# Kernel tuning notes

Measured on AMD Instinct MI355X. Metric: run time of the kernel, lower is better.

## Reference

```python
import jax, jax.numpy as jnp
import numpy as np

N = 268  # nodes per graph (4288 / nhid=16)


def _cheb_norm(edge_index, edge_weight):
    # PyG ChebConv normalization with normalization='sym', lambda_max=2.0:
    # L_hat = (2/lambda_max) * L - I = -D^{-1/2} A D^{-1/2} (diagonal cancels to 0)
    row, col = edge_index[0], edge_index[1]
    deg = jax.ops.segment_sum(edge_weight, row, num_segments=N)
    dis = jnp.where(deg > 0, jax.lax.rsqrt(deg), 0.0)
    return -edge_weight * dis[row] * dis[col]


def _cheb_conv(x, edge_index, norm, w, b):
    # K=2: out = T0 @ W0 + T1 @ W1 + b,  T0 = x, T1 = L_hat x
    row, col = edge_index[0], edge_index[1]
    tx1 = jax.ops.segment_sum(norm[:, None] * x[col], row, num_segments=N)
    return x @ w[0] + tx1 @ w[1] + b


def _forward_single(x, edge_index, edge_attr, gc1_w, gc1_b, gc4_w, gc4_b):
    norm = _cheb_norm(edge_index, edge_attr)
    h = jax.nn.relu(_cheb_conv(x, edge_index, norm, gc1_w, gc1_b))
    # dropout in eval mode -> identity
    return _cheb_conv(h, edge_index, norm, gc4_w, gc4_b)  # [N, nhid]


def setup_inputs() -> dict:
    key = jax.random.key(0)
    ks = jax.random.split(key, 20)
    B, E, F, H = 64, 8576, 268, 16
    inp = {}
    for i, nm in enumerate(['x1', 'x2', 'x3']):
        inp[nm] = jax.random.normal(ks[i], (B, N, F), dtype=jnp.float32)
    for i, nm in enumerate(['edge_index1', 'edge_index2', 'edge_index3']):
        inp[nm] = jax.random.randint(ks[3 + i], (B, 2, E), 0, N)
    for i, nm in enumerate(['edge_attr1', 'edge_attr2', 'edge_attr3']):
        inp[nm] = jax.random.uniform(ks[6 + i], (B, E), dtype=jnp.float32)
    s = 0.05
    inp['gc1_w'] = jax.random.normal(ks[9], (2, F, H), dtype=jnp.float32) * s
    inp['gc1_b'] = jnp.zeros((H,), dtype=jnp.float32)
    inp['gc4_w'] = jax.random.normal(ks[10], (2, H, H), dtype=jnp.float32) * s
    inp['gc4_b'] = jnp.zeros((H,), dtype=jnp.float32)
    inp['fc1_w'] = jax.random.normal(ks[11], (1024, N * H), dtype=jnp.float32) * s
    inp['fc1_b'] = jnp.zeros((1024,), dtype=jnp.float32)
    inp['fc2_w'] = jax.random.normal(ks[12], (512, 1024), dtype=jnp.float32) * s
    inp['fc2_b'] = jnp.zeros((512,), dtype=jnp.float32)
    return inp


def reference(x1, x2, x3, edge_index1, edge_index2, edge_index3,
              edge_attr1, edge_attr2, edge_attr3,
              gc1_w, gc1_b, gc4_w, gc4_b, fc1_w, fc1_b, fc2_w, fc2_b):
    conv = jax.vmap(_forward_single, in_axes=(0, 0, 0, None, None, None, None))

    def branch(x, ei, ea):
        c = conv(x, ei, ea, gc1_w, gc1_b, gc4_w, gc4_b)      # [B, N, H]
        f = c.reshape(c.shape[0], -1)                        # [B, 4288]
        h = jax.nn.relu(f @ fc1_w.T + fc1_b)                 # classifier dropout: eval -> id
        return h @ fc2_w.T + fc2_b                           # [B, 512]

    return (branch(x1, edge_index1, edge_attr1),
            branch(x2, edge_index2, edge_attr2),
            branch(x3, edge_index3, edge_attr3))
```

## Files before the change

### kernel.cpp

```cpp
#include <hip/hip_runtime.h>


#define NN   268
#define EE   8576
#define NG   192
#define FDIM 4288
#define CONVT 1024

typedef __bf16 bf16_t;
typedef bf16_t bf16x8 __attribute__((ext_vector_type(8)));
typedef bf16_t bf16x4 __attribute__((ext_vector_type(4)));
typedef float  f32x4  __attribute__((ext_vector_type(4)));

#define WB_OFF   0
#define FB_OFF   2195456
#define WXT_OFF  (FB_OFF + 411648)
#define H1_OFF   (WXT_OFF + 4608)
#define R1P_OFF  (H1_OFF + 196608)
#define R2P_OFF  (R1P_OFF + 1572864)

#define NCASTB 2144

__global__ __launch_bounds__(256) void k_prep(
    const float* __restrict__ fc1w, const float* __restrict__ gc1w,
    bf16_t* __restrict__ wbf, bf16_t* __restrict__ wxt)
{
    if (blockIdx.x < NCASTB) {
        const int t = blockIdx.x * 256 + threadIdx.x;
        const int lane = t & 63;
        const int rest = t >> 6;
        const int n = (rest / 134) * 16 + (lane & 15);
        const int k = (rest % 134) * 32 + (lane >> 4) * 8;
        const float4 a = *(const float4*)(fc1w + (size_t)n * FDIM + k);
        const float4 b = *(const float4*)(fc1w + (size_t)n * FDIM + k + 4);
        bf16x8 v;
        v[0] = (bf16_t)a.x; v[1] = (bf16_t)a.y; v[2] = (bf16_t)a.z; v[3] = (bf16_t)a.w;
        v[4] = (bf16_t)b.x; v[5] = (bf16_t)b.y; v[6] = (bf16_t)b.z; v[7] = (bf16_t)b.w;
        *(bf16x8*)(wbf + (size_t)t * 8) = v;
    } else {
        for (int idx = threadIdx.x; idx < 2 * 9 * 64; idx += 256) {
            const int lane = idx & 63, chunk = (idx >> 6) % 9, nt = idx / (9 * 64);
            const int n = lane & 15, q = lane >> 4;
            bf16x8 v;
#pragma unroll
            for (int j = 0; j < 8; ++j) {
                const int k = chunk * 32 + q * 8 + j;
                v[j] = (k < NN) ? (bf16_t)gc1w[nt * FDIM + k * 16 + n] : (bf16_t)0.f;
            }
            *(bf16x8*)(wxt + (size_t)idx * 8) = v;
        }
    }
}

__global__ __launch_bounds__(CONVT) void k_conv(
    const float* __restrict__ x0, const float* __restrict__ x1, const float* __restrict__ x2,
    const int* __restrict__ ei0, const int* __restrict__ ei1, const int* __restrict__ ei2,
    const float* __restrict__ ea0, const float* __restrict__ ea1, const float* __restrict__ ea2,
    const bf16_t* __restrict__ wxt,
    const float* __restrict__ gc1b, const float* __restrict__ gc4w,
    const float* __restrict__ gc4b, bf16_t* __restrict__ fout)
{
    const int g = blockIdx.x;
    const int br = g >> 6, b = g & 63;
    const float* xg = ((br == 0) ? x0 : (br == 1) ? x1 : x2) + (size_t)b * (NN * NN);
    const int*   ei = (br == 0) ? ei0 : (br == 1) ? ei1 : ei2;
    const float* ea = (br == 0) ? ea0 : (br == 1) ? ea1 : ea2;
    const int*   rowp = ei + (size_t)b * (2 * EE);
    const int*   colp = rowp + EE;
    const float* eap  = ea + (size_t)b * EE;

    __shared__ unsigned int e_s[EE];
    __shared__ __align__(16) bf16_t A_s[FDIM];
    __shared__ __align__(16) bf16_t S_s[FDIM];
    __shared__ __align__(16) float  xw0_s[FDIM];
    __shared__ float degS[NN];
    __shared__ int   cntS[NN];
    __shared__ int   offS[NN + 1];
    __shared__ int   curS[NN];
    __shared__ float w4_s[512];
    __shared__ float b1_s[16];
    __shared__ float b4_s[16];
    const int tid = threadIdx.x;
    const int lane = tid & 63, wid = tid >> 6;

    if (tid < NN) { degS[tid] = 0.f; cntS[tid] = 0; }
    if (tid < 512) w4_s[tid] = gc4w[tid];
    if (tid < 16) { b1_s[tid] = gc1b[tid]; b4_s[tid] = gc4b[tid]; }

    {
        const int q = lane >> 4, nlo = lane & 15;
        for (int mt = wid; mt < 17; mt += 16) {
            const int mrow = mt * 16 + nlo;
            const bool mvalid = (mrow < NN);
            const float* xrow = xg + (size_t)mrow * NN;
            f32x4 acc0 = {0.f, 0.f, 0.f, 0.f}, acc1 = {0.f, 0.f, 0.f, 0.f};
            for (int ch = 0; ch < 9; ++ch) {
                const int k0 = ch * 32 + q * 8;
                float4 p0 = make_float4(0.f, 0.f, 0.f, 0.f);
                float4 p1 = make_float4(0.f, 0.f, 0.f, 0.f);
                if (mvalid) {
                    if (k0 < NN)     p0 = *(const float4*)(xrow + k0);
                    if (k0 + 4 < NN) p1 = *(const float4*)(xrow + k0 + 4);
                }
                bf16x8 a;
                a[0] = (bf16_t)p0.x; a[1] = (bf16_t)p0.y; a[2] = (bf16_t)p0.z; a[3] = (bf16_t)p0.w;
                a[4] = (bf16_t)p1.x; a[5] = (bf16_t)p1.y; a[6] = (bf16_t)p1.z; a[7] = (bf16_t)p1.w;
                const bf16x8 b0 = *(const bf16x8*)(wxt + (size_t)(ch * 64 + lane) * 8);
                const bf16x8 b1 = *(const bf16x8*)(wxt + (size_t)(576 + ch * 64 + lane) * 8);
                acc0 = __builtin_amdgcn_mfma_f32_16x16x32_bf16(a, b0, acc0, 0, 0, 0);
                acc1 = __builtin_amdgcn_mfma_f32_16x16x32_bf16(a, b1, acc1, 0, 0, 0);
            }
#pragma unroll
            for (int r = 0; r < 4; ++r) {
                const int row = mt * 16 + q * 4 + r;
                if (row < NN) {
                    xw0_s[row * 16 + nlo] = acc0[r];
                    A_s[row * 16 + nlo] = (bf16_t)acc1[r];
                }
            }
        }
    }
    __syncthreads();

    for (int e = tid; e < EE; e += CONVT) {
        const int r = rowp[e];
        atomicAdd(&degS[r], eap[e]);
        atomicAdd(&cntS[r], 1);
    }
    for (int st = 1; st < NN; st <<= 1) {
        __syncthreads();
        int v = 0;
        if (tid < NN) { v = cntS[tid]; if (tid >= st) v += cntS[tid - st]; }
        __syncthreads();
        if (tid < NN) cntS[tid] = v;
    }
    __syncthreads();
    if (tid < NN) offS[tid + 1] = cntS[tid];
    if (tid == 0) offS[0] = 0;
    __syncthreads();
    if (tid < NN) {
        curS[tid] = offS[tid];
        const float d = degS[tid];
        degS[tid] = (d > 0.f) ? rsqrtf(d) : 0.f;
    }
    __syncthreads();
    for (int e = tid; e < EE; e += CONVT) {
        const int r = rowp[e], c = colp[e];
        const float nv = -eap[e] * degS[r] * degS[c];
        union { float f; unsigned u; } cv; cv.f = nv;
        const unsigned bits = (cv.u + 0x7fffu + ((cv.u >> 16) & 1u)) >> 16;
        const int pos = atomicAdd(&curS[r], 1);
        e_s[pos] = ((unsigned)c << 16) | bits;
    }
    __syncthreads();

    const int j4 = tid & 3, nl = tid >> 2;
    const bf16x4* A4 = (const bf16x4*)A_s;

    for (int n = nl; n < NN; n += 256) {
        const int s = offS[n], e = offS[n + 1];
        const f32x4 xv = *(const f32x4*)&xw0_s[n * 16 + j4 * 4];
        float ax = 0.f, ay = 0.f, az = 0.f, aw = 0.f;
        int i = s;
        for (; i + 3 < e; i += 4) {
            const unsigned p0 = e_s[i], p1 = e_s[i + 1], p2 = e_s[i + 2], p3 = e_s[i + 3];
            const float w0 = __uint_as_float(p0 << 16);
            const float w1 = __uint_as_float(p1 << 16);
            const float w2 = __uint_as_float(p2 << 16);
            const float w3 = __uint_as_float(p3 << 16);
            const bf16x4 a0 = A4[(p0 >> 16) * 4 + j4];
            const bf16x4 a1 = A4[(p1 >> 16) * 4 + j4];
            const bf16x4 a2 = A4[(p2 >> 16) * 4 + j4];
            const bf16x4 a3 = A4[(p3 >> 16) * 4 + j4];
            ax += w0 * (float)a0[0] + w1 * (float)a1[0] + w2 * (float)a2[0] + w3 * (float)a3[0];
            ay += w0 * (float)a0[1] + w1 * (float)a1[1] + w2 * (float)a2[1] + w3 * (float)a3[1];
            az += w0 * (float)a0[2] + w1 * (float)a1[2] + w2 * (float)a2[2] + w3 * (float)a3[2];
            aw += w0 * (float)a0[3] + w1 * (float)a1[3] + w2 * (float)a2[3] + w3 * (float)a3[3];
        }
        for (; i < e; ++i) {
            const unsigned p0 = e_s[i];
            const float w0 = __uint_as_float(p0 << 16);
            const bf16x4 a0 = A4[(p0 >> 16) * 4 + j4];
            ax += w0 * (float)a0[0]; ay += w0 * (float)a0[1];
            az += w0 * (float)a0[2]; aw += w0 * (float)a0[3];
        }
        bf16x4 h;
        h[0] = (bf16_t)fmaxf(xv[0] + ax + b1_s[j4 * 4 + 0], 0.f);
        h[1] = (bf16_t)fmaxf(xv[1] + ay + b1_s[j4 * 4 + 1], 0.f);
        h[2] = (bf16_t)fmaxf(xv[2] + az + b1_s[j4 * 4 + 2], 0.f);
        h[3] = (bf16_t)fmaxf(xv[3] + aw + b1_s[j4 * 4 + 3], 0.f);
        *(bf16x4*)&S_s[n * 16 + j4 * 4] = h;
    }
    __syncthreads();

    for (int idx = tid; idx < FDIM; idx += CONVT) {
        const int n = idx >> 4, j = idx & 15;
        const bf16x8 s0 = *(const bf16x8*)&S_s[n * 16];
        const bf16x8 s1 = *(const bf16x8*)&S_s[n * 16 + 8];
        float a1 = 0.f;
#pragma unroll
        for (int k = 0; k < 8; ++k) a1 += (float)s0[k] * w4_s[256 + k * 16 + j];
#pragma unroll
        for (int k = 0; k < 8; ++k) a1 += (float)s1[k] * w4_s[256 + (k + 8) * 16 + j];
        A_s[idx] = (bf16_t)a1;
    }
    __syncthreads();

    for (int n = nl; n < NN; n += 256) {
        const int s = offS[n], e = offS[n + 1];
        float ax = 0.f, ay = 0.f, az = 0.f, aw = 0.f;
        int i = s;
        for (; i + 3 < e; i += 4) {
            const unsigned p0 = e_s[i], p1 = e_s[i + 1], p2 = e_s[i + 2], p3 = e_s[i + 3];
            const float w0 = __uint_as_float(p0 << 16);
            const float w1 = __uint_as_float(p1 << 16);
            const float w2 = __uint_as_float(p2 << 16);
            const float w3 = __uint_as_float(p3 << 16);
            const bf16x4 a0 = A4[(p0 >> 16) * 4 + j4];
            const bf16x4 a1 = A4[(p1 >> 16) * 4 + j4];
            const bf16x4 a2 = A4[(p2 >> 16) * 4 + j4];
            const bf16x4 a3 = A4[(p3 >> 16) * 4 + j4];
            ax += w0 * (float)a0[0] + w1 * (float)a1[0] + w2 * (float)a2[0] + w3 * (float)a3[0];
            ay += w0 * (float)a0[1] + w1 * (float)a1[1] + w2 * (float)a2[1] + w3 * (float)a3[1];
            az += w0 * (float)a0[2] + w1 * (float)a1[2] + w2 * (float)a2[2] + w3 * (float)a3[2];
            aw += w0 * (float)a0[3] + w1 * (float)a1[3] + w2 * (float)a2[3] + w3 * (float)a3[3];
        }
        for (; i < e; ++i) {
            const unsigned p0 = e_s[i];
            const float w0 = __uint_as_float(p0 << 16);
            const bf16x4 a0 = A4[(p0 >> 16) * 4 + j4];
            ax += w0 * (float)a0[0]; ay += w0 * (float)a0[1];
            az += w0 * (float)a0[2]; aw += w0 * (float)a0[3];
        }
        float h0[4];
#pragma unroll
        for (int c2 = 0; c2 < 4; ++c2) h0[c2] = b4_s[j4 * 4 + c2];
        const bf16x8 s0 = *(const bf16x8*)&S_s[n * 16];
        const bf16x8 s1 = *(const bf16x8*)&S_s[n * 16 + 8];
#pragma unroll
        for (int k = 0; k < 8; ++k) {
            const float sv = (float)s0[k];
#pragma unroll
            for (int c2 = 0; c2 < 4; ++c2) h0[c2] += sv * w4_s[k * 16 + j4 * 4 + c2];
        }
#pragma unroll
        for (int k = 0; k < 8; ++k) {
            const float sv = (float)s1[k];
#pragma unroll
            for (int c2 = 0; c2 < 4; ++c2) h0[c2] += sv * w4_s[(k + 8) * 16 + j4 * 4 + c2];
        }
        bf16x4 o;
        o[0] = (bf16_t)(h0[0] + ax); o[1] = (bf16_t)(h0[1] + ay);
        o[2] = (bf16_t)(h0[2] + az); o[3] = (bf16_t)(h0[3] + aw);
        *(bf16x4*)(fout + (size_t)g * FDIM + n * 16 + j4 * 4) = o;
    }
}

__global__ __launch_bounds__(256) void k_fc1(
    const bf16_t* __restrict__ fb, const bf16_t* __restrict__ wbf, float* __restrict__ r1p)
{
    const int mt = blockIdx.x, nb = blockIdx.y, kz = blockIdx.z;
    const int wid = threadIdx.x >> 6, lane = threadIdx.x & 63;
    const int q = lane >> 4, nlo = lane & 15;
    const int n0 = nb * 128 + wid * 32;
    const int cstart = kz * 17;
    const int ccnt   = (kz == 7) ? 15 : 17;

    const bf16_t* arow = fb + (size_t)(mt * 16 + nlo) * FDIM + q * 8;
    const int nt0 = nb * 8 + wid * 2;
    f32x4 acc[2];
#pragma unroll
    for (int t = 0; t < 2; ++t) { acc[t][0]=0.f; acc[t][1]=0.f; acc[t][2]=0.f; acc[t][3]=0.f; }

    for (int ch = 0; ch < ccnt; ++ch) {
        const size_t ko = (size_t)(cstart + ch) * 32;
        const bf16x8 a = *(const bf16x8*)(arow + ko);
#pragma unroll
        for (int t = 0; t < 2; ++t) {
            const bf16x8 bv = *(const bf16x8*)(
                wbf + (((size_t)(nt0 + t) * 134 + cstart + ch) * 64 + lane) * 8);
            acc[t] = __builtin_amdgcn_mfma_f32_16x16x32_bf16(a, bv, acc[t], 0, 0, 0);
        }
    }
    float* outp = r1p + (size_t)kz * (NG * 1024);
#pragma unroll
    for (int t = 0; t < 2; ++t)
#pragma unroll
        for (int r = 0; r < 4; ++r)
            outp[(size_t)(mt * 16 + q * 4 + r) * 1024 + n0 + t * 16 + nlo] = acc[t][r];
}

__global__ __launch_bounds__(256) void k_red1(
    const float* __restrict__ r1p, const float* __restrict__ b1, float* __restrict__ h1)
{
    const size_t i = ((size_t)blockIdx.x * 256 + threadIdx.x) * 4;
    const size_t S = (size_t)NG * 1024;
    float4 s = *(const float4*)(r1p + i);
#pragma unroll
    for (int k = 1; k < 8; ++k) {
        const float4 t = *(const float4*)(r1p + (size_t)k * S + i);
        s.x += t.x; s.y += t.y; s.z += t.z; s.w += t.w;
    }
    const float4 bb = *(const float4*)(b1 + (i & 1023));
    float4 o;
    o.x = fmaxf(s.x + bb.x, 0.f);
    o.y = fmaxf(s.y + bb.y, 0.f);
    o.z = fmaxf(s.z + bb.z, 0.f);
    o.w = fmaxf(s.w + bb.w, 0.f);
    *(float4*)(h1 + i) = o;
}

__global__ __launch_bounds__(256) void k_fc2(
    const float* __restrict__ h1, const float* __restrict__ w2, float* __restrict__ r2p)
{
    const int m0 = blockIdx.x * 64;
    const int n0 = blockIdx.y * 64;
    const int kb = blockIdx.z * 64;
    __shared__ float rs[64][68];
    __shared__ float wss[64][68];
    const int tid = threadIdx.x;
    const int mt = tid & 15, nt = tid >> 4;
    float acc[4][4];
#pragma unroll
    for (int i = 0; i < 4; ++i)
#pragma unroll
        for (int j = 0; j < 4; ++j) acc[i][j] = 0.f;

    for (int idx = tid; idx < 1024; idx += 256) {
        const int r = idx >> 4, qq = idx & 15;
        const int gk = kb + qq * 4;
        *(float4*)&rs[r][qq * 4]  = *(const float4*)(h1 + (size_t)(m0 + r) * 1024 + gk);
        *(float4*)&wss[r][qq * 4] = *(const float4*)(w2 + (size_t)(n0 + r) * 1024 + gk);
    }
    __syncthreads();
    for (int kq = 0; kq < 16; ++kq) {
        float4 av[4], bv[4];
#pragma unroll
        for (int i = 0; i < 4; ++i) av[i] = *(const float4*)&rs[mt + 16 * i][kq * 4];
#pragma unroll
        for (int j = 0; j < 4; ++j) bv[j] = *(const float4*)&wss[nt + 16 * j][kq * 4];
#pragma unroll
        for (int i = 0; i < 4; ++i)
#pragma unroll
            for (int j = 0; j < 4; ++j)
                acc[i][j] += av[i].x * bv[j].x + av[i].y * bv[j].y +
                             av[i].z * bv[j].z + av[i].w * bv[j].w;
    }
    float* outp = r2p + (size_t)blockIdx.z * (NG * 512);
#pragma unroll
    for (int i = 0; i < 4; ++i)
#pragma unroll
        for (int j = 0; j < 4; ++j)
            outp[(size_t)(m0 + mt + 16 * i) * 512 + n0 + nt + 16 * j] = acc[i][j];
}

__global__ __launch_bounds__(256) void k_red2(
    const float* __restrict__ r2p, const float* __restrict__ b2, float* __restrict__ out)
{
    const size_t i = ((size_t)blockIdx.x * 256 + threadIdx.x) * 4;
    const size_t S = (size_t)NG * 512;
    float4 s = *(const float4*)(r2p + i);
#pragma unroll
    for (int k = 1; k < 16; ++k) {
        const float4 t = *(const float4*)(r2p + (size_t)k * S + i);
        s.x += t.x; s.y += t.y; s.z += t.z; s.w += t.w;
    }
    const float4 bb = *(const float4*)(b2 + (i & 511));
    s.x += bb.x; s.y += bb.y; s.z += bb.z; s.w += bb.w;
    *(float4*)(out + i) = s;
}

extern "C" void kernel_launch(void* const* d_in, const int* in_sizes, int n_in,
                              void* d_out, int out_size, void* d_ws, size_t ws_size,
                              hipStream_t stream)
{
    const float* x0   = (const float*)d_in[0];
    const float* x1   = (const float*)d_in[1];
    const float* x2   = (const float*)d_in[2];
    const int*   ei0  = (const int*)d_in[3];
    const int*   ei1  = (const int*)d_in[4];
    const int*   ei2  = (const int*)d_in[5];
    const float* ea0  = (const float*)d_in[6];
    const float* ea1  = (const float*)d_in[7];
    const float* ea2  = (const float*)d_in[8];
    const float* gc1w = (const float*)d_in[9];
    const float* gc1b = (const float*)d_in[10];
    const float* gc4w = (const float*)d_in[11];
    const float* gc4b = (const float*)d_in[12];
    const float* fc1w = (const float*)d_in[13];
    const float* fc1b = (const float*)d_in[14];
    const float* fc2w = (const float*)d_in[15];
    const float* fc2b = (const float*)d_in[16];

    float*  ws  = (float*)d_ws;
    bf16_t* wbf = (bf16_t*)(ws + WB_OFF);
    bf16_t* fb  = (bf16_t*)(ws + FB_OFF);
    bf16_t* wxt = (bf16_t*)(ws + WXT_OFF);
    float*  h1  = ws + H1_OFF;
    float*  r1p = ws + R1P_OFF;
    float*  r2p = ws + R2P_OFF;
    float*  out = (float*)d_out;

    k_prep<<<NCASTB + 1, 256, 0, stream>>>(fc1w, gc1w, wbf, wxt);
    k_conv<<<NG, CONVT, 0, stream>>>(x0, x1, x2, ei0, ei1, ei2, ea0, ea1, ea2,
                                     wxt, gc1b, gc4w, gc4b, fb);
    k_fc1 <<<dim3(12, 8, 8), 256, 0, stream>>>(fb, wbf, r1p);
    k_red1<<<NG, 256, 0, stream>>>(r1p, fc1b, h1);
    k_fc2 <<<dim3(3, 8, 16), 256, 0, stream>>>(h1, fc2w, r2p);
    k_red2<<<96, 256, 0, stream>>>(r2p, fc2b, out);
}
```

Before: 212.0 us.

## Double-buffer x tile loads via global_load_lds with swizzle, stage weights in LDS

```diff
diff --git a/kernel.cpp b/kernel.cpp
--- a/kernel.cpp
+++ b/kernel.cpp
@@ -20,6 +20,12 @@
 #define R2P_OFF  (R1P_OFF + 1572864)
 
 #define NCASTB 2144
+
+__device__ __forceinline__ void gload_lds16(const float* g, float* l) {
+    __builtin_amdgcn_global_load_lds(
+        (const __attribute__((address_space(1))) void*)g,
+        (__attribute__((address_space(3))) void*)l, 16, 0, 0);
+}
 
 __global__ __launch_bounds__(256) void k_prep(
     const float* __restrict__ fc1w, const float* __restrict__ gc1w,
@@ -69,10 +75,13 @@
     const int*   colp = rowp + EE;
     const float* eap  = ea + (size_t)b * EE;
 
-    __shared__ unsigned int e_s[EE];
+    __shared__ __align__(16) unsigned char u0_s[16 * 1024 * 4];
+    unsigned int* e_s = (unsigned int*)u0_s;
+    float* xsl = (float*)u0_s;
     __shared__ __align__(16) bf16_t A_s[FDIM];
     __shared__ __align__(16) bf16_t S_s[FDIM];
     __shared__ __align__(16) float  xw0_s[FDIM];
+    __shared__ __align__(16) bf16_t wxt_s[9216];
     __shared__ float degS[NN];
     __shared__ int   cntS[NN];
     __shared__ int   offS[NN + 1];
@@ -83,39 +92,67 @@
     const int tid = threadIdx.x;
     const int lane = tid & 63, wid = tid >> 6;
 
+    {
+        const bf16x8* src = (const bf16x8*)wxt;
+        bf16x8* dst = (bf16x8*)wxt_s;
+        for (int i = tid; i < 1152; i += CONVT) dst[i] = src[i];
+    }
     if (tid < NN) { degS[tid] = 0.f; cntS[tid] = 0; }
     if (tid < 512) w4_s[tid] = gc4w[tid];
     if (tid < 16) { b1_s[tid] = gc1b[tid]; b4_s[tid] = gc4b[tid]; }
+    __syncthreads();
 
     {
-        const int q = lane >> 4, nlo = lane & 15;
+        const int m = lane & 15, q = lane >> 4;
+        const int rsub  = lane >> 3;
+        const int sphys = lane & 7;
+        const int sgl   = sphys ^ rsub;
+        float* slab = xsl + (size_t)wid * 1024;
+
         for (int mt = wid; mt < 17; mt += 16) {
-            const int mrow = mt * 16 + nlo;
-            const bool mvalid = (mrow < NN);
-            const float* xrow = xg + (size_t)mrow * NN;
+            int grow0 = mt * 16 + rsub;
+            int grow1 = mt * 16 + 8 + rsub;
+            if (grow0 >= NN) grow0 = 0;
+            if (grow1 >= NN) grow1 = 0;
+            const float* rb0 = xg + (size_t)grow0 * NN;
+            const float* rb1 = xg + (size_t)grow1 * NN;
+
+#define XW_ISSUE(ch, bb) do {                                   \
+            int kc_ = (ch) * 32 + sgl * 4;                      \
+            if (kc_ + 4 > NN) kc_ = 0;   \
+            gload_lds16(rb0 + kc_, slab + (bb) * 512);          \
+            gload_lds16(rb1 + kc_, slab + (bb) * 512 + 256);    \
+        } while (0)
+
+            XW_ISSUE(0, 0);
+            XW_ISSUE(1, 1);
             f32x4 acc0 = {0.f, 0.f, 0.f, 0.f}, acc1 = {0.f, 0.f, 0.f, 0.f};
+#pragma unroll
             for (int ch = 0; ch < 9; ++ch) {
-                const int k0 = ch * 32 + q * 8;
-                float4 p0 = make_float4(0.f, 0.f, 0.f, 0.f);
-                float4 p1 = make_float4(0.f, 0.f, 0.f, 0.f);
-                if (mvalid) {
-                    if (k0 < NN)     p0 = *(const float4*)(xrow + k0);
-                    if (k0 + 4 < NN) p1 = *(const float4*)(xrow + k0 + 4);
-                }
+                const int bb = ch & 1;
+                if (ch < 8) { asm volatile("s_waitcnt vmcnt(2)" ::: "memory"); }
+                else        { asm volatile("s_waitcnt vmcnt(0)" ::: "memory"); }
+                const float* bp = slab + bb * 512 + m * 32;
+                const int c0 = (((q * 2)     ^ (m & 7)) * 4);
+                const int c1 = (((q * 2 + 1) ^ (m & 7)) * 4);
+                const f32x4 lo = *(const f32x4*)(bp + c0);
+                const f32x4 hi = *(const f32x4*)(bp + c1);
                 bf16x8 a;
-                a[0] = (bf16_t)p0.x; a[1] = (bf16_t)p0.y; a[2] = (bf16_t)p0.z; a[3] = (bf16_t)p0.w;
-                a[4] = (bf16_t)p1.x; a[5] = (bf16_t)p1.y; a[6] = (bf16_t)p1.z; a[7] = (bf16_t)p1.w;
-                const bf16x8 b0 = *(const bf16x8*)(wxt + (size_t)(ch * 64 + lane) * 8);
-                const bf16x8 b1 = *(const bf16x8*)(wxt + (size_t)(576 + ch * 64 + lane) * 8);
+                a[0] = (bf16_t)lo[0]; a[1] = (bf16_t)lo[1]; a[2] = (bf16_t)lo[2]; a[3] = (bf16_t)lo[3];
+                a[4] = (bf16_t)hi[0]; a[5] = (bf16_t)hi[1]; a[6] = (bf16_t)hi[2]; a[7] = (bf16_t)hi[3];
+                const bf16x8 b0 = *(const bf16x8*)&wxt_s[(size_t)(ch * 64 + lane) * 8];
+                const bf16x8 b1 = *(const bf16x8*)&wxt_s[(size_t)(576 + ch * 64 + lane) * 8];
                 acc0 = __builtin_amdgcn_mfma_f32_16x16x32_bf16(a, b0, acc0, 0, 0, 0);
                 acc1 = __builtin_amdgcn_mfma_f32_16x16x32_bf16(a, b1, acc1, 0, 0, 0);
+                if (ch + 2 <= 8) XW_ISSUE(ch + 2, bb);
             }
+#undef XW_ISSUE
 #pragma unroll
             for (int r = 0; r < 4; ++r) {
                 const int row = mt * 16 + q * 4 + r;
                 if (row < NN) {
-                    xw0_s[row * 16 + nlo] = acc0[r];
-                    A_s[row * 16 + nlo] = (bf16_t)acc1[r];
+                    xw0_s[row * 16 + m] = acc0[r];
+                    A_s[row * 16 + m] = (bf16_t)acc1[r];
                 }
             }
         }
```

Measured after the change: 217.3 us. +2.5%, slower.

## Merge weight-cast prep kernel into conv kernel as extra blocks

Applied to the files above, without the earlier changes.

```diff
diff --git a/kernel.cpp b/kernel.cpp
--- a/kernel.cpp
+++ b/kernel.cpp
@@ -6,6 +6,7 @@
 #define NG   192
 #define FDIM 4288
 #define CONVT 1024
+#define NCAST 536
 
 typedef __bf16 bf16_t;
 typedef bf16_t bf16x8 __attribute__((ext_vector_type(8)));
@@ -14,19 +15,34 @@
 
 #define WB_OFF   0
 #define FB_OFF   2195456
-#define WXT_OFF  (FB_OFF + 411648)
-#define H1_OFF   (WXT_OFF + 4608)
+#define H1_OFF   (FB_OFF + 411648)
 #define R1P_OFF  (H1_OFF + 196608)
 #define R2P_OFF  (R1P_OFF + 1572864)
 
-#define NCASTB 2144
-
-__global__ __launch_bounds__(256) void k_prep(
+__global__ __launch_bounds__(CONVT) void k_main(
+    const float* __restrict__ x0, const float* __restrict__ x1, const float* __restrict__ x2,
+    const int* __restrict__ ei0, const int* __restrict__ ei1, const int* __restrict__ ei2,
+    const float* __restrict__ ea0, const float* __restrict__ ea1, const float* __restrict__ ea2,
     const float* __restrict__ fc1w, const float* __restrict__ gc1w,
-    bf16_t* __restrict__ wbf, bf16_t* __restrict__ wxt)
-{
-    if (blockIdx.x < NCASTB) {
-        const int t = blockIdx.x * 256 + threadIdx.x;
+    const float* __restrict__ gc1b, const float* __restrict__ gc4w,
+    const float* __restrict__ gc4b, bf16_t* __restrict__ wbf, bf16_t* __restrict__ fout)
+{
+    __shared__ unsigned int e_s[EE];
+    __shared__ __align__(16) bf16_t A_s[FDIM];
+    __shared__ __align__(16) bf16_t S_s[FDIM];
+    __shared__ __align__(16) float  xw0_s[FDIM];
+    __shared__ __align__(16) bf16_t wxt_s[9216];
+    __shared__ float degS[NN];
+    __shared__ int   cntS[NN];
+    __shared__ int   offS[NN + 1];
+    __shared__ int   curS[NN];
+    __shared__ float w4_s[512];
+    __shared__ float b1_s[16];
+    __shared__ float b4_s[16];
+    const int tid = threadIdx.x;
+
+    if (blockIdx.x >= NG) {
+        const int t = (blockIdx.x - NG) * CONVT + tid;
         const int lane = t & 63;
         const int rest = t >> 6;
         const int n = (rest / 134) * 16 + (lane & 15);
@@ -37,29 +53,9 @@
         v[0] = (bf16_t)a.x; v[1] = (bf16_t)a.y; v[2] = (bf16_t)a.z; v[3] = (bf16_t)a.w;
         v[4] = (bf16_t)b.x; v[5] = (bf16_t)b.y; v[6] = (bf16_t)b.z; v[7] = (bf16_t)b.w;
         *(bf16x8*)(wbf + (size_t)t * 8) = v;
-    } else {
-        for (int idx = threadIdx.x; idx < 2 * 9 * 64; idx += 256) {
-            const int lane = idx & 63, chunk = (idx >> 6) % 9, nt = idx / (9 * 64);
-            const int n = lane & 15, q = lane >> 4;
-            bf16x8 v;
-#pragma unroll
-            for (int j = 0; j < 8; ++j) {
-                const int k = chunk * 32 + q * 8 + j;
-                v[j] = (k < NN) ? (bf16_t)gc1w[nt * FDIM + k * 16 + n] : (bf16_t)0.f;
-            }
-            *(bf16x8*)(wxt + (size_t)idx * 8) = v;
-        }
-    }
-}
-
-__global__ __launch_bounds__(CONVT) void k_conv(
-    const float* __restrict__ x0, const float* __restrict__ x1, const float* __restrict__ x2,
-    const int* __restrict__ ei0, const int* __restrict__ ei1, const int* __restrict__ ei2,
-    const float* __restrict__ ea0, const float* __restrict__ ea1, const float* __restrict__ ea2,
-    const bf16_t* __restrict__ wxt,
-    const float* __restrict__ gc1b, const float* __restrict__ gc4w,
-    const float* __restrict__ gc4b, bf16_t* __restrict__ fout)
-{
+        return;
+    }
+
     const int g = blockIdx.x;
     const int br = g >> 6, b = g & 63;
     const float* xg = ((br == 0) ? x0 : (br == 1) ? x1 : x2) + (size_t)b * (NN * NN);
@@ -68,24 +64,23 @@
     const int*   rowp = ei + (size_t)b * (2 * EE);
     const int*   colp = rowp + EE;
     const float* eap  = ea + (size_t)b * EE;
-
-    __shared__ unsigned int e_s[EE];
-    __shared__ __align__(16) bf16_t A_s[FDIM];
-    __shared__ __align__(16) bf16_t S_s[FDIM];
-    __shared__ __align__(16) float  xw0_s[FDIM];
-    __shared__ float degS[NN];
-    __shared__ int   cntS[NN];
-    __shared__ int   offS[NN + 1];
-    __shared__ int   curS[NN];
-    __shared__ float w4_s[512];
-    __shared__ float b1_s[16];
-    __shared__ float b4_s[16];
-    const int tid = threadIdx.x;
     const int lane = tid & 63, wid = tid >> 6;
 
+    for (int idx = tid; idx < 2 * 9 * 64; idx += CONVT) {
+        const int l = idx & 63, chunk = (idx >> 6) % 9, nt = idx / (9 * 64);
+        const int n = l & 15, q = l >> 4;
+        bf16x8 v;
+#pragma unroll
+        for (int j = 0; j < 8; ++j) {
+            const int k = chunk * 32 + q * 8 + j;
+            v[j] = (k < NN) ? (bf16_t)gc1w[nt * FDIM + k * 16 + n] : (bf16_t)0.f;
+        }
+        *(bf16x8*)&wxt_s[(size_t)idx * 8] = v;
+    }
     if (tid < NN) { degS[tid] = 0.f; cntS[tid] = 0; }
     if (tid < 512) w4_s[tid] = gc4w[tid];
     if (tid < 16) { b1_s[tid] = gc1b[tid]; b4_s[tid] = gc4b[tid]; }
+    __syncthreads();
 
     {
         const int q = lane >> 4, nlo = lane & 15;
@@ -105,8 +100,8 @@
                 bf16x8 a;
                 a[0] = (bf16_t)p0.x; a[1] = (bf16_t)p0.y; a[2] = (bf16_t)p0.z; a[3] = (bf16_t)p0.w;
                 a[4] = (bf16_t)p1.x; a[5] = (bf16_t)p1.y; a[6] = (bf16_t)p1.z; a[7] = (bf16_t)p1.w;
-                const bf16x8 b0 = *(const bf16x8*)(wxt + (size_t)(ch * 64 + lane) * 8);
-                const bf16x8 b1 = *(const bf16x8*)(wxt + (size_t)(576 + ch * 64 + lane) * 8);
+                const bf16x8 b0 = *(const bf16x8*)&wxt_s[(size_t)(ch * 64 + lane) * 8];
+                const bf16x8 b1 = *(const bf16x8*)&wxt_s[(size_t)(576 + ch * 64 + lane) * 8];
                 acc0 = __builtin_amdgcn_mfma_f32_16x16x32_bf16(a, b0, acc0, 0, 0, 0);
                 acc1 = __builtin_amdgcn_mfma_f32_16x16x32_bf16(a, b1, acc1, 0, 0, 0);
             }
@@ -395,15 +390,14 @@
     float*  ws  = (float*)d_ws;
     bf16_t* wbf = (bf16_t*)(ws + WB_OFF);
     bf16_t* fb  = (bf16_t*)(ws + FB_OFF);
-    bf16_t* wxt = (bf16_t*)(ws + WXT_OFF);
     float*  h1  = ws + H1_OFF;
     float*  r1p = ws + R1P_OFF;
     float*  r2p = ws + R2P_OFF;
     float*  out = (float*)d_out;
 
-    k_prep<<<NCASTB + 1, 256, 0, stream>>>(fc1w, gc1w, wbf, wxt);
-    k_conv<<<NG, CONVT, 0, stream>>>(x0, x1, x2, ei0, ei1, ei2, ea0, ea1, ea2,
-                                     wxt, gc1b, gc4w, gc4b, fb);
+    k_main<<<NG + NCAST, CONVT, 0, stream>>>(x0, x1, x2, ei0, ei1, ei2,
+                                             ea0, ea1, ea2, fc1w, gc1w,
+                                             gc1b, gc4w, gc4b, wbf, fb);
     k_fc1 <<<dim3(12, 8, 8), 256, 0, stream>>>(fb, wbf, r1p);
     k_red1<<<NG, 256, 0, stream>>>(r1p, fc1b, h1);
     k_fc2 <<<dim3(3, 8, 16), 256, 0, stream>>>(h1, fc2w, r2p);
```

Measured after the change: 203.4 us. 1.04x faster.
